# Kernel optimization log

Measured on AMD Instinct MI355X. Metric: run time of the kernel, lower is better.

## Reference

```python
import jax, jax.numpy as jnp
import numpy as np

# --- static config (mirrors init_kwargs / letter_code) ---
BATCH, NODES, AMINO, ATOM = 64, 512, 64, 32
NTYPES = 20
# heavy-atom count minus 1 for the 20 standard amino acids (ARNDCQEGHILKMFPSTWYV)
RES_LENS = np.array([4, 10, 7, 7, 5, 8, 8, 3, 9, 7, 7, 8, 7, 10, 6, 5, 6, 13, 11, 6])
RMAX = int(RES_LENS.max())  # 13


def setup_inputs() -> dict:
    rng = np.random.default_rng(0)
    type_ids = rng.integers(0, NTYPES, size=NODES)           # metadata.seq as type indices
    lens = RES_LENS[type_ids]                                 # residue lengths per node
    valid = np.arange(RMAX)[None, :] < lens[:, None]          # (NODES, RMAX) valid-atom mask
    gather_idx = np.nonzero(valid.reshape(-1))[0]             # flat indices of real atoms

    key = jax.random.key(0)
    k1, k2 = jax.random.split(key)
    x = jax.random.normal(k1, (BATCH, NODES, AMINO, 3), dtype=jnp.float32)
    # stacked per-type TensLinear weights, zero-padded to RMAX residues of output
    W = jax.random.normal(k2, (NTYPES, AMINO, RMAX * ATOM), dtype=jnp.float32) * 0.05
    wmask = (np.arange(RMAX)[None, :, None] < RES_LENS[:, None, None])  # (NTYPES, RMAX, 1)
    wmask = np.broadcast_to(wmask, (NTYPES, RMAX, ATOM)).reshape(NTYPES, 1, RMAX * ATOM)
    W = W * jnp.asarray(wmask, dtype=jnp.float32)
    return {
        "x": x,
        "W": W,
        "type_ids": jnp.asarray(type_ids, dtype=jnp.int64),
        "gather_idx": jnp.asarray(gather_idx, dtype=jnp.int64),
    }


def reference(x, W, type_ids, gather_idx):
    # x: (B, N, amino, 3); W: (T, amino, RMAX*atom); equivariant linear on amino axis
    batch, nodes = x.shape[0], x.shape[1]
    Wg = W[type_ids]                                   # (N, amino, RMAX*atom) type dispatch
    out = jnp.einsum('bnav,naj->bnjv', x, Wg)          # (B, N, RMAX*atom, 3)
    out = out.reshape(batch, nodes * RMAX, ATOM, 3)    # padded per-residue atom blocks
    return out[:, gather_idx]                          # (B, total_atoms, atom, 3) = torch.cat
```

## Files before the change

kernel.cpp:

```cpp
#include <hip/hip_runtime.h>

typedef __bf16 bf16;
typedef __bf16 bf16x8 __attribute__((ext_vector_type(8)));
typedef float f32x4 __attribute__((ext_vector_type(4)));
typedef unsigned short u16;
typedef u16 u16x8 __attribute__((ext_vector_type(8)));
typedef unsigned int u32;

#define BATCH 64
#define NODES 512
#define AMINO 64
#define NTYPES 20
#define RMAX 13
#define NJT 26
#define PADA 72

__constant__ int c_res_lens[NTYPES] = {4,10,7,7,5,8,8,3,9,7,7,8,7,10,6,5,6,13,11,6};

__device__ __forceinline__ u16 f2bf(float f) {
    u32 u; __builtin_memcpy(&u, &f, 4);
    u32 r = u + 0x7FFFu + ((u >> 16) & 1u);
    return (u16)(r >> 16);
}

__device__ __forceinline__ int detect_i64(const int* __restrict__ p) {
    int z = 0;
#pragma unroll
    for (int k = 0; k < 16; ++k) z |= p[2 * k + 1];
    return z == 0;
}
__device__ __forceinline__ int tid_at(const int* __restrict__ p, int n, int is64) {
    return p[is64 ? 2 * n : n];
}

__global__ __launch_bounds__(256) void prep_kernel(const float* __restrict__ W,
                                                   const int* __restrict__ type_ids,
                                                   u16* __restrict__ wswz,
                                                   int* __restrict__ S) {
    if (blockIdx.x < 260) {
        int g = blockIdx.x * 256 + threadIdx.x;
        if (g >= NTYPES * NJT * 2 * 64) return;
        int lane = g & 63;
        int chunk = g >> 6;
        int kh = chunk & 1;
        int tj = chunk >> 1;
        int t = tj / NJT;
        int jt = tj - t * NJT;
        int q = lane >> 4, c = lane & 15;
        int a0 = kh * 32 + q * 8;
        int j = jt * 16 + c;
        u16x8 v;
#pragma unroll
        for (int i = 0; i < 8; ++i)
            v[i] = f2bf(W[(size_t)(t * AMINO + a0 + i) * (RMAX * 32) + j]);
        *(u16x8*)(wswz + (size_t)chunk * 512 + lane * 8) = v;
    } else {
        __shared__ int s[256];
        int is64 = detect_i64(type_ids);
        int i = threadIdx.x;
        int la = c_res_lens[tid_at(type_ids, 2 * i, is64)];
        int lb = c_res_lens[tid_at(type_ids, 2 * i + 1, is64)];
        s[i] = la + lb;
        __syncthreads();
        for (int off = 1; off < 256; off <<= 1) {
            int v = (i >= off) ? s[i - off] : 0;
            __syncthreads();
            s[i] += v;
            __syncthreads();
        }
        int excl = s[i] - (la + lb);
        S[2 * i] = excl;
        S[2 * i + 1] = excl + la;
    }
}

__global__ __launch_bounds__(256) void main_kernel(const float* __restrict__ x,
                                                   const int* __restrict__ type_ids,
                                                   const int* __restrict__ S,
                                                   const u16* __restrict__ wswz,
                                                   float* __restrict__ out,
                                                   int G) {
    __shared__ __align__(16) u16 planes[3][16][PADA];

    const int bid = blockIdx.x;
    const int n = bid >> 2;
    const int m = bid & 3;
    const int tid = threadIdx.x;
    const int w = tid >> 6;
    const int l = tid & 63;

    const int is64 = detect_i64(type_ids);
    const int t = tid_at(type_ids, n, is64);
    const int len = c_res_lens[t];
    const int s0 = S[n];

#pragma unroll
    for (int i = 0; i < 4; ++i) {
        int b16 = i * 4 + w;
        const float* src = x + ((size_t)(m * 16 + b16) * NODES + n) * 192 + l * 3;
        float v0 = src[0];
        float v1 = src[1];
        float v2 = src[2];
        planes[0][b16][l] = f2bf(v0);
        planes[1][b16][l] = f2bf(v1);
        planes[2][b16][l] = f2bf(v2);
    }
    __syncthreads();

    const int q = l >> 4;
    const int c = l & 15;

    union Frag { u16x8 u; bf16x8 b; };
    Frag Af[3][2];
#pragma unroll
    for (int v = 0; v < 3; ++v)
#pragma unroll
        for (int kh = 0; kh < 2; ++kh)
            Af[v][kh].u = *(const u16x8*)(&planes[v][c][kh * 32 + q * 8]);

    for (int r = w; r < len; r += 4) {
        Frag Bf[2][2];
#pragma unroll
        for (int jj = 0; jj < 2; ++jj)
#pragma unroll
            for (int kh = 0; kh < 2; ++kh)
                Bf[jj][kh].u = *(const u16x8*)(wswz +
                                (size_t)((t * NJT + (2 * r + jj)) * 2 + kh) * 512 + l * 8);

        const int g = s0 + r;

        f32x4 acc[2][3];
        const f32x4 z = {0.f, 0.f, 0.f, 0.f};
#pragma unroll
        for (int jj = 0; jj < 2; ++jj)
#pragma unroll
            for (int v = 0; v < 3; ++v) {
                f32x4 a0 = __builtin_amdgcn_mfma_f32_16x16x32_bf16(Af[v][0].b, Bf[jj][0].b, z, 0, 0, 0);
                acc[jj][v] = __builtin_amdgcn_mfma_f32_16x16x32_bf16(Af[v][1].b, Bf[jj][1].b, a0, 0, 0, 0);
            }

#pragma unroll
        for (int reg = 0; reg < 4; ++reg) {
            float* rowp = out + ((size_t)(m * 16 + q * 4 + reg) * G + g) * 96;
#pragma unroll
            for (int jj = 0; jj < 2; ++jj) {
                float* p = rowp + (jj * 16 + c) * 3;
                p[0] = acc[jj][0][reg];
                p[1] = acc[jj][1][reg];
                p[2] = acc[jj][2][reg];
            }
        }
    }
}

extern "C" void kernel_launch(void* const* d_in, const int* in_sizes, int n_in,
                              void* d_out, int out_size, void* d_ws, size_t ws_size,
                              hipStream_t stream) {
    const float* x = (const float*)d_in[0];
    const float* W = (const float*)d_in[1];
    const int* type_ids = (const int*)d_in[2];
    int G = out_size / (BATCH * 32 * 3);

    int* S = (int*)d_ws;
    u16* wswz = (u16*)((char*)d_ws + 4096);

    prep_kernel<<<261, 256, 0, stream>>>(W, type_ids, wswz, S);
    main_kernel<<<NODES * 4, 256, 0, stream>>>(x, type_ids, S, wswz, (float*)d_out, G);
}
```

Baseline: 127.6 us.

## Load x fragments directly into registers and pack per-node metadata

The main kernel now builds its MFMA A-fragments by reading x with vectorized 16-byte global loads straight into registers and converting to bf16 there. This removes the shared-memory staging buffer and its barrier, but each wave now redundantly loads the same x tile. Type id, residue length and output offset are packed into one int in the prep kernel, which removes the int64 detection and the extra global reads from main_kernel. Output stores are expressed as a 12-byte memcpy so the compiler may merge them.

```diff
diff --git a/kernel.cpp b/kernel.cpp
--- a/kernel.cpp
+++ b/kernel.cpp
@@ -13,7 +13,6 @@
 #define NTYPES 20
 #define RMAX 13
 #define NJT 26
-#define PADA 72
 
 __constant__ int c_res_lens[NTYPES] = {4,10,7,7,5,8,8,3,9,7,7,8,7,10,6,5,6,13,11,6};
 
@@ -36,7 +35,7 @@
 __global__ __launch_bounds__(256) void prep_kernel(const float* __restrict__ W,
                                                    const int* __restrict__ type_ids,
                                                    u16* __restrict__ wswz,
-                                                   int* __restrict__ S) {
+                                                   int* __restrict__ meta) {
     if (blockIdx.x < 260) {
         int g = blockIdx.x * 256 + threadIdx.x;
         if (g >= NTYPES * NJT * 2 * 64) return;
@@ -58,8 +57,10 @@
         __shared__ int s[256];
         int is64 = detect_i64(type_ids);
         int i = threadIdx.x;
-        int la = c_res_lens[tid_at(type_ids, 2 * i, is64)];
-        int lb = c_res_lens[tid_at(type_ids, 2 * i + 1, is64)];
+        int t0 = tid_at(type_ids, 2 * i, is64);
+        int t1 = tid_at(type_ids, 2 * i + 1, is64);
+        int la = c_res_lens[t0];
+        int lb = c_res_lens[t1];
         s[i] = la + lb;
         __syncthreads();
         for (int off = 1; off < 256; off <<= 1) {
@@ -69,54 +70,49 @@
             __syncthreads();
         }
         int excl = s[i] - (la + lb);
-        S[2 * i] = excl;
-        S[2 * i + 1] = excl + la;
+        meta[2 * i]     = t0 | (la << 5) | (excl << 9);
+        meta[2 * i + 1] = t1 | (lb << 5) | ((excl + la) << 9);
     }
 }
 
 __global__ __launch_bounds__(256) void main_kernel(const float* __restrict__ x,
-                                                   const int* __restrict__ type_ids,
-                                                   const int* __restrict__ S,
+                                                   const int* __restrict__ meta,
                                                    const u16* __restrict__ wswz,
                                                    float* __restrict__ out,
                                                    int G) {
-    __shared__ __align__(16) u16 planes[3][16][PADA];
-
     const int bid = blockIdx.x;
     const int n = bid >> 2;
     const int m = bid & 3;
     const int tid = threadIdx.x;
     const int w = tid >> 6;
     const int l = tid & 63;
-
-    const int is64 = detect_i64(type_ids);
-    const int t = tid_at(type_ids, n, is64);
-    const int len = c_res_lens[t];
-    const int s0 = S[n];
-
-#pragma unroll
-    for (int i = 0; i < 4; ++i) {
-        int b16 = i * 4 + w;
-        const float* src = x + ((size_t)(m * 16 + b16) * NODES + n) * 192 + l * 3;
-        float v0 = src[0];
-        float v1 = src[1];
-        float v2 = src[2];
-        planes[0][b16][l] = f2bf(v0);
-        planes[1][b16][l] = f2bf(v1);
-        planes[2][b16][l] = f2bf(v2);
-    }
-    __syncthreads();
-
     const int q = l >> 4;
     const int c = l & 15;
 
+    const int mt = meta[n];
+    const int t = mt & 31;
+    const int len = (mt >> 5) & 15;
+    const int s0 = mt >> 9;
+
     union Frag { u16x8 u; bf16x8 b; };
     Frag Af[3][2];
+    {
+        const float* base = x + ((size_t)(m * 16 + c) * NODES + n) * 192;
 #pragma unroll
-    for (int v = 0; v < 3; ++v)
+        for (int kh = 0; kh < 2; ++kh) {
+            f32x4 xv[6];
+            const float* src = base + (kh * 32 + q * 8) * 3;
 #pragma unroll
-        for (int kh = 0; kh < 2; ++kh)
-            Af[v][kh].u = *(const u16x8*)(&planes[v][c][kh * 32 + q * 8]);
+            for (int i6 = 0; i6 < 6; ++i6)
+                xv[i6] = *(const f32x4*)(src + i6 * 4);
+            const float* f = (const float*)xv;
+#pragma unroll
+            for (int v = 0; v < 3; ++v)
+#pragma unroll
+                for (int i = 0; i < 8; ++i)
+                    Af[v][kh].u[i] = f2bf(f[i * 3 + v]);
+        }
+    }
 
     for (int r = w; r < len; r += 4) {
         Frag Bf[2][2];
@@ -144,10 +140,8 @@
             float* rowp = out + ((size_t)(m * 16 + q * 4 + reg) * G + g) * 96;
 #pragma unroll
             for (int jj = 0; jj < 2; ++jj) {
-                float* p = rowp + (jj * 16 + c) * 3;
-                p[0] = acc[jj][0][reg];
-                p[1] = acc[jj][1][reg];
-                p[2] = acc[jj][2][reg];
+                float tmp[3] = {acc[jj][0][reg], acc[jj][1][reg], acc[jj][2][reg]};
+                __builtin_memcpy(rowp + (jj * 16 + c) * 3, tmp, 12);
             }
         }
     }
@@ -161,9 +155,9 @@
     const int* type_ids = (const int*)d_in[2];
     int G = out_size / (BATCH * 32 * 3);
 
-    int* S = (int*)d_ws;
+    int* meta = (int*)d_ws;
     u16* wswz = (u16*)((char*)d_ws + 4096);
 
-    prep_kernel<<<261, 256, 0, stream>>>(W, type_ids, wswz, S);
-    main_kernel<<<NODES * 4, 256, 0, stream>>>(x, type_ids, S, wswz, (float*)d_out, G);
+    prep_kernel<<<261, 256, 0, stream>>>(W, type_ids, wswz, meta);
+    main_kernel<<<NODES * 4, 256, 0, stream>>>(x, meta, wswz, (float*)d_out, G);
 }
```

Result: slower. 132.9 us (+4.2%).
